# Kernel optimization log

Hardware: AMD Instinct MI355X
Metric: run time of the kernel (lower is better)

The kernel has to match this reference:

```python
import jax, jax.numpy as jnp
import numpy as np
import math

D = 1024      # hidden_size
H = 16        # num_heads
HD = D // H   # head_dim = 64
ROPE = 64     # rope_dim == head_dim (full-head rotation, empty pass-through)
E = 8         # num_experts
F = 2560
BASE = 10000.0
EPS = 1e-5
SPECIALS = jnp.arange(2, 8)  # special_tokens indices {2..7} used as global tokens


def _ln(x, w, b):
    m = x.mean(-1, keepdims=True)
    v = x.var(-1, keepdims=True)  # biased var, matches torch LayerNorm
    return (x - m) / jnp.sqrt(v + EPS) * w + b


def _rope(x, cos, sin):
    # x: [B,H,T,HD]; rotate first ROPE dims via half-split (NOT rotate-half interleave)
    x1, x2 = x[..., : ROPE // 2], x[..., ROPE // 2 : ROPE]
    rot = jnp.concatenate([x1 * cos - x2 * sin, x1 * sin + x2 * cos], axis=-1)
    return jnp.concatenate([rot, x[..., ROPE:]], axis=-1)


def setup_inputs() -> dict:
    key = jax.random.key(0)
    ks = jax.random.split(key, 8)
    B, T = 1, 1024
    g = lambda k, shape, s: (jax.random.normal(k, shape, jnp.float32) * s)
    return {
        "x": g(ks[0], (B, T, D), 1.0),
        "input_ids": jax.random.randint(ks[1], (B, T), 0, 32000),
        "ln1_w": jnp.ones((D,), jnp.float32), "ln1_b": jnp.zeros((D,), jnp.float32),
        "qkv_w": g(ks[2], (D, 3 * D), 0.02), "qkv_b": jnp.zeros((3 * D,), jnp.float32),
        "attn_out_w": g(ks[3], (D, D), 0.02), "attn_out_b": jnp.zeros((D,), jnp.float32),
        "ln2_w": jnp.ones((D,), jnp.float32), "ln2_b": jnp.zeros((D,), jnp.float32),
        "gate_w": g(ks[4], (D, E), 0.02), "gate_b": jnp.zeros((E,), jnp.float32),
        "fc_w": g(ks[5], (E, D, 2 * F), 0.02), "fc_b": jnp.zeros((E, 2 * F), jnp.float32),
        "eout_w": g(ks[6], (E, F, D), 0.02), "eout_b": jnp.zeros((E, D), jnp.float32),
    }


def _block(x, input_ids, ln1_w, ln1_b, qkv_w, qkv_b, attn_out_w, attn_out_b,
           ln2_w, ln2_b, gate_w, gate_b, fc_w, fc_b, eout_w, eout_b):
    B, T, _ = x.shape
    # --- self-attention (pre-norm) ---
    h = _ln(x, ln1_w, ln1_b)
    qkv = h @ qkv_w + qkv_b
    q, k, v = jnp.split(qkv, 3, axis=-1)
    resh = lambda t: t.reshape(B, T, H, HD).transpose(0, 2, 1, 3)  # [B,H,T,HD]
    q, k, v = resh(q), resh(k), resh(v)
    pos = jnp.arange(T, dtype=jnp.float32)
    inv = 1.0 / (BASE ** (jnp.arange(0, ROPE, 2, dtype=jnp.float32) / ROPE))
    fr = pos[:, None] * inv[None, :]            # [T, ROPE/2]
    cos, sin = jnp.cos(fr), jnp.sin(fr)
    q = _rope(q, cos, sin)
    k = _rope(k, cos, sin)
    causal = jnp.tril(jnp.ones((T, T), bool))
    glob = (input_ids[..., None] == SPECIALS).any(-1)            # [B,T]
    allowed = causal[None, None] | glob[:, None, :, None]        # [B,1,T,T]
    logits = jnp.einsum('bhqd,bhkd->bhqk', q, k) / math.sqrt(HD)
    neg = -jnp.finfo(logits.dtype).max
    logits = jnp.where(allowed, logits, neg)
    aw = jax.nn.softmax(logits, axis=-1)
    attn = jnp.einsum('bhqk,bhkd->bhqd', aw, v).transpose(0, 2, 1, 3).reshape(B, T, H * HD)
    x = x + (attn @ attn_out_w + attn_out_b)
    # --- MoE GEGLU FFN (hard top-1 routing) ---
    h2 = _ln(x, ln2_w, ln2_b)
    gp = jax.nn.softmax(h2 @ gate_w + gate_b, axis=-1)           # [B,T,E]
    gw = gp.max(-1)
    gi = gp.argmax(-1)
    xf = h2.reshape(-1, D)
    gif = gi.reshape(-1)
    gwf = gw.reshape(-1)
    N = xf.shape[0]
    outf = jnp.zeros((N, D), x.dtype)
    for e in range(E):  # fixed small expert loop; select by routing mask
        h12 = xf @ fc_w[e] + fc_b[e]
        x1, x2 = h12[:, :F], h12[:, F:]
        y = (x1 * jax.nn.gelu(x2, approximate=False)) @ eout_w[e] + eout_b[e]
        outf = outf + jnp.where((gif == e)[:, None], y, 0.0)
    outf = outf * gwf[:, None]
    sums = jax.ops.segment_sum(gwf, gif, num_segments=E)
    counts = jax.ops.segment_sum(jnp.ones_like(gwf), gif, num_segments=E)
    usage = sums / (counts + 1e-8)
    moe_loss = jnp.sum((usage - 1.0 / E) ** 2)
    return x + outf.reshape(B, T, D), moe_loss


def reference(x, input_ids, ln1_w, ln1_b, qkv_w, qkv_b, attn_out_w, attn_out_b,
              ln2_w, ln2_b, gate_w, gate_b, fc_w, fc_b, eout_w, eout_b):
    return _block(x, input_ids, ln1_w, ln1_b, qkv_w, qkv_b, attn_out_w, attn_out_b,
                  ln2_w, ln2_b, gate_w, gate_b, fc_w, fc_b, eout_w, eout_b)
```

## Files before the change

kernel.cpp:

```cpp
#include <hip/hip_runtime.h>
#include <float.h>
#include <math.h>
#include <stdint.h>

#define T_ 1024
#define D_ 1024
#define H_ 16
#define HD_ 64
#define E_ 8
#define F_ 2560
#define D3_ 3072
#define F2_ 5120

#define WS_H    0u
#define WS_QKV  1048576u
#define WS_ATTN 4194304u
#define WS_X2   5242880u
#define WS_H2   6291456u
#define WS_A    7340032u
#define WS_GW   9961472u
#define WS_GI   9962496u
#define WS_OFFS 9963520u
#define WS_PERM 9963536u

typedef short short8 __attribute__((ext_vector_type(8)));
typedef short short4v __attribute__((ext_vector_type(4)));
typedef __bf16 bf16x8 __attribute__((ext_vector_type(8)));
typedef float floatx4 __attribute__((ext_vector_type(4)));

union FragU { short8 s; bf16x8 b; };

__device__ __forceinline__ short f2bf(float f) {
    union { float f; uint32_t u; } a; a.f = f;
    uint32_t r = a.u + 0x7fffu + ((a.u >> 16) & 1u);
    return (short)(r >> 16);
}

__device__ __forceinline__ void cvt16(const float4& a0, const float4& a1,
                                      const float4& a2, const float4& a3,
                                      short8& c0, short8& c1) {
    c0[0]=f2bf(a0.x); c0[1]=f2bf(a0.y); c0[2]=f2bf(a0.z); c0[3]=f2bf(a0.w);
    c0[4]=f2bf(a1.x); c0[5]=f2bf(a1.y); c0[6]=f2bf(a1.z); c0[7]=f2bf(a1.w);
    c1[0]=f2bf(a2.x); c1[1]=f2bf(a2.y); c1[2]=f2bf(a2.z); c1[3]=f2bf(a2.w);
    c1[4]=f2bf(a3.x); c1[5]=f2bf(a3.y); c1[6]=f2bf(a3.z); c1[7]=f2bf(a3.w);
}

#define GEMM_IDS \
    const int tid  = threadIdx.x;                 \
    const int a_m  = tid >> 1;                    \
    const int a_kh = (tid & 1) * 16;              \
    const int lane = tid & 63, wave = tid >> 6;   \
    const int wm = wave & 1,  wn = wave >> 1;     \
    const int quad = lane >> 4, lm = lane & 15;

__global__ __launch_bounds__(256) void gemm_mfma_full(
    const float* __restrict__ A, int lda,
    const float* __restrict__ B, int ldb,
    const float* __restrict__ bias,
    float* __restrict__ C, int ldc, int K)
{
    __shared__ __align__(16) short As[4*128*8];
    __shared__ __align__(16) short Bs[64*40];
    const int row0 = blockIdx.y * 128, col0 = blockIdx.x * 64;
    GEMM_IDS
    const int b_n = tid >> 2, b_kc = tid & 3;
    floatx4 acc[4][2];
    #pragma unroll
    for (int i=0;i<4;i++)
        #pragma unroll
        for (int j=0;j<2;j++) acc[i][j] = (floatx4){0.f,0.f,0.f,0.f};

    const float* apx = A + (size_t)(row0 + a_m) * lda + a_kh;
    const float* bpx = B + (size_t)(b_kc*8) * ldb + col0 + b_n;
    const int kcA = (tid & 1) * 2;

    float4 a0, a1, a2, a3; float bvv[8];
    a0 = *(const float4*)(apx);     a1 = *(const float4*)(apx + 4);
    a2 = *(const float4*)(apx + 8); a3 = *(const float4*)(apx + 12);
    #pragma unroll
    for (int j=0;j<8;j++) bvv[j] = bpx[(size_t)j*ldb];

    for (int k0 = 0; k0 < K; k0 += 32) {
        __syncthreads();
        short8 c0, c1, cb;
        cvt16(a0,a1,a2,a3,c0,c1);
        #pragma unroll
        for (int j=0;j<8;j++) cb[j] = f2bf(bvv[j]);
        *(short8*)&As[((kcA  )*128 + a_m)*8] = c0;
        *(short8*)&As[((kcA+1)*128 + a_m)*8] = c1;
        *(short8*)&Bs[b_n*40 + b_kc*8] = cb;
        __syncthreads();
        if (k0 + 32 < K) {
            const float* ap2 = apx + k0 + 32;
            a0 = *(const float4*)(ap2);     a1 = *(const float4*)(ap2 + 4);
            a2 = *(const float4*)(ap2 + 8); a3 = *(const float4*)(ap2 + 12);
            const float* bp2 = bpx + (size_t)(k0+32) * ldb;
            #pragma unroll
            for (int j=0;j<8;j++) bvv[j] = bp2[(size_t)j*ldb];
        }
        FragU fa[4], fb[2];
        #pragma unroll
        for (int i=0;i<4;i++) fa[i].s = *(short8*)&As[(quad*128 + wm*64 + i*16 + lm)*8];
        #pragma unroll
        for (int j=0;j<2;j++) fb[j].s = *(short8*)&Bs[(wn*32 + j*16 + lm)*40 + quad*8];
        #pragma unroll
        for (int i=0;i<4;i++)
            #pragma unroll
            for (int j=0;j<2;j++)
                acc[i][j] = __builtin_amdgcn_mfma_f32_16x16x32_bf16(fa[i].b, fb[j].b, acc[i][j], 0,0,0);
    }
    #pragma unroll
    for (int i=0;i<4;i++)
        #pragma unroll
        for (int j=0;j<2;j++) {
            int col = col0 + wn*32 + j*16 + lm;
            float bb = bias ? bias[col] : 0.f;
            #pragma unroll
            for (int r=0;r<4;r++) {
                int row = row0 + wm*64 + i*16 + quad*4 + r;
                C[(size_t)row*ldc + col] = acc[i][j][r] + bb;
            }
        }
}

__global__ __launch_bounds__(256) void gemm_mfma_acc(
    const float* __restrict__ A, int lda,
    const float* __restrict__ B, int ldb, long sB,
    const int* __restrict__ offs, const int* __restrict__ perm,
    float* __restrict__ Cacc, int ldc, int K, int nsk)
{
    const int sk = blockIdx.z % nsk;
    const int e  = blockIdx.z / nsk;
    int off = 0, Ne = T_;
    if (offs) { off = offs[e]; Ne = offs[e+1] - off; }
    const int row0 = blockIdx.y * 128;
    if (row0 >= Ne) return;
    const int col0 = blockIdx.x * 64;
    B += (long)e * sB;

    __shared__ __align__(16) short As[4*128*8];
    __shared__ __align__(16) short Bs[64*40];
    __shared__ int toks[128];
    GEMM_IDS
    const int b_n = tid >> 2, b_kc = tid & 3;
    if (tid < 128) {
        int r = row0 + tid;
        toks[tid] = offs ? ((r < Ne) ? perm[off + r] : -1) : r;
    }
    __syncthreads();

    floatx4 acc[4][2];
    #pragma unroll
    for (int i=0;i<4;i++)
        #pragma unroll
        for (int j=0;j<2;j++) acc[i][j] = (floatx4){0.f,0.f,0.f,0.f};

    const int tokA = toks[a_m];
    const float* apx = (tokA >= 0) ? (A + (size_t)tokA * lda + a_kh) : nullptr;
    const float* bpx = B + (size_t)(b_kc*8) * ldb + col0 + b_n;
    const int kcA = (tid & 1) * 2;
    const int Kp = K / nsk;
    const int koff = sk * Kp, kend = koff + Kp;

    float4 a0, a1, a2, a3; float bvv[8];
    a0 = make_float4(0,0,0,0); a1 = a0; a2 = a0; a3 = a0;
    if (apx) {
        a0 = *(const float4*)(apx + koff);     a1 = *(const float4*)(apx + koff + 4);
        a2 = *(const float4*)(apx + koff + 8); a3 = *(const float4*)(apx + koff + 12);
    }
    {
        const float* bp2 = bpx + (size_t)koff * ldb;
        #pragma unroll
        for (int j=0;j<8;j++) bvv[j] = bp2[(size_t)j*ldb];
    }

    for (int k0 = koff; k0 < kend; k0 += 32) {
        __syncthreads();
        short8 c0, c1, cb;
        cvt16(a0,a1,a2,a3,c0,c1);
        #pragma unroll
        for (int j=0;j<8;j++) cb[j] = f2bf(bvv[j]);
        *(short8*)&As[((kcA  )*128 + a_m)*8] = c0;
        *(short8*)&As[((kcA+1)*128 + a_m)*8] = c1;
        *(short8*)&Bs[b_n*40 + b_kc*8] = cb;
        __syncthreads();
        if (k0 + 32 < kend) {
            if (apx) {
                const float* ap2 = apx + k0 + 32;
                a0 = *(const float4*)(ap2);     a1 = *(const float4*)(ap2 + 4);
                a2 = *(const float4*)(ap2 + 8); a3 = *(const float4*)(ap2 + 12);
            }
            const float* bp2 = bpx + (size_t)(k0+32) * ldb;
            #pragma unroll
            for (int j=0;j<8;j++) bvv[j] = bp2[(size_t)j*ldb];
        }
        FragU fa[4], fb[2];
        #pragma unroll
        for (int i=0;i<4;i++) fa[i].s = *(short8*)&As[(quad*128 + wm*64 + i*16 + lm)*8];
        #pragma unroll
        for (int j=0;j<2;j++) fb[j].s = *(short8*)&Bs[(wn*32 + j*16 + lm)*40 + quad*8];
        #pragma unroll
        for (int i=0;i<4;i++)
            #pragma unroll
            for (int j=0;j<2;j++)
                acc[i][j] = __builtin_amdgcn_mfma_f32_16x16x32_bf16(fa[i].b, fb[j].b, acc[i][j], 0,0,0);
    }
    #pragma unroll
    for (int i=0;i<4;i++)
        #pragma unroll
        for (int j=0;j<2;j++) {
            int col = col0 + wn*32 + j*16 + lm;
            #pragma unroll
            for (int r=0;r<4;r++) {
                int tk = toks[wm*64 + i*16 + quad*4 + r];
                if (tk >= 0) atomicAdd(&Cacc[(size_t)tk*ldc + col], acc[i][j][r]);
            }
        }
}

__global__ __launch_bounds__(256) void moe_fc_mfma(
    const float* __restrict__ h2, const float* __restrict__ fcw,
    const float* __restrict__ fcb, const int* __restrict__ offs,
    const int* __restrict__ perm, float* __restrict__ aout)
{
    const int e = blockIdx.z;
    const int off = offs[e];
    const int Ne = offs[e+1] - off;
    const int row0 = blockIdx.y * 128;
    if (row0 >= Ne) return;
    const int col0 = blockIdx.x * 32;

    __shared__ __align__(16) short As[4*128*8];
    __shared__ __align__(16) short B1s[32*40];
    __shared__ __align__(16) short B2s[32*40];
    __shared__ int toks[128];
    GEMM_IDS
    const int n_l = tid & 31, kg = tid >> 5;
    if (tid < 128) {
        int r = row0 + tid;
        toks[tid] = (r < Ne) ? perm[off + r] : -1;
    }
    __syncthreads();

    floatx4 acc1[4], acc2[4];
    #pragma unroll
    for (int i=0;i<4;i++) {
        acc1[i] = (floatx4){0.f,0.f,0.f,0.f};
        acc2[i] = (floatx4){0.f,0.f,0.f,0.f};
    }

    const float* W = fcw + (size_t)e * D_ * F2_;
    const int tokA = toks[a_m];
    const float* apx = (tokA >= 0) ? (h2 + (size_t)tokA * D_ + a_kh) : nullptr;
    const float* bpx = W + (size_t)(kg*4) * F2_ + col0 + n_l;
    const int kcA = (tid & 1) * 2;

    float4 a0, a1, a2, a3; float b1v[4], b2v[4];
    a0 = make_float4(0,0,0,0); a1 = a0; a2 = a0; a3 = a0;
    if (apx) {
        a0 = *(const float4*)(apx);     a1 = *(const float4*)(apx + 4);
        a2 = *(const float4*)(apx + 8); a3 = *(const float4*)(apx + 12);
    }
    #pragma unroll
    for (int j=0;j<4;j++) { b1v[j] = bpx[(size_t)j*F2_]; b2v[j] = bpx[(size_t)j*F2_ + F_]; }

    for (int k0 = 0; k0 < D_; k0 += 32) {
        __syncthreads();
        short8 c0, c1;
        short4v cb1, cb2;
        cvt16(a0,a1,a2,a3,c0,c1);
        #pragma unroll
        for (int j=0;j<4;j++) { cb1[j] = f2bf(b1v[j]); cb2[j] = f2bf(b2v[j]); }
        *(short8*)&As[((kcA  )*128 + a_m)*8] = c0;
        *(short8*)&As[((kcA+1)*128 + a_m)*8] = c1;
        *(short4v*)&B1s[n_l*40 + kg*4] = cb1;
        *(short4v*)&B2s[n_l*40 + kg*4] = cb2;
        __syncthreads();
        if (k0 + 32 < D_) {
            if (apx) {
                const float* ap2 = apx + k0 + 32;
                a0 = *(const float4*)(ap2);     a1 = *(const float4*)(ap2 + 4);
                a2 = *(const float4*)(ap2 + 8); a3 = *(const float4*)(ap2 + 12);
            }
            const float* bp2 = bpx + (size_t)(k0+32) * F2_;
            #pragma unroll
            for (int j=0;j<4;j++) { b1v[j] = bp2[(size_t)j*F2_]; b2v[j] = bp2[(size_t)j*F2_ + F_]; }
        }
        FragU fa[4], fb1, fb2;
        #pragma unroll
        for (int i=0;i<4;i++) fa[i].s = *(short8*)&As[(quad*128 + wm*64 + i*16 + lm)*8];
        fb1.s = *(short8*)&B1s[(wn*16 + lm)*40 + quad*8];
        fb2.s = *(short8*)&B2s[(wn*16 + lm)*40 + quad*8];
        #pragma unroll
        for (int i=0;i<4;i++) {
            acc1[i] = __builtin_amdgcn_mfma_f32_16x16x32_bf16(fa[i].b, fb1.b, acc1[i], 0,0,0);
            acc2[i] = __builtin_amdgcn_mfma_f32_16x16x32_bf16(fa[i].b, fb2.b, acc2[i], 0,0,0);
        }
    }
    {
        int col = col0 + wn*16 + lm;
        float b1 = fcb[(size_t)e*F2_ + col];
        float b2 = fcb[(size_t)e*F2_ + F_ + col];
        #pragma unroll
        for (int i=0;i<4;i++)
            #pragma unroll
            for (int r=0;r<4;r++) {
                int tk = toks[wm*64 + i*16 + quad*4 + r];
                if (tk < 0) continue;
                float v1 = acc1[i][r] + b1;
                float v2 = acc2[i][r] + b2;
                float g = v2 * 0.5f * (1.0f + erff(v2 * 0.70710678118654752f));
                aout[(size_t)tk*F_ + col] = v1 * g;
            }
    }
}

__global__ __launch_bounds__(128) void flash_attn(
    const float* __restrict__ qkv, const int* __restrict__ ids,
    float* __restrict__ attnout)
{
    const int h  = blockIdx.y;
    const int q0 = blockIdx.x * 32;
    const int tid = threadIdx.x;
    const int lane = tid & 63, w = tid >> 6;
    const int quad = lane >> 4, lm = lane & 15;

    __shared__ __align__(16) short Qs[32*72];
    __shared__ __align__(16) short Ks[64*72];
    __shared__ __align__(16) short Vt[64*72];
    __shared__ __align__(16) short Ps[2][16*72];
    __shared__ int globf[32];

    {
        int row = tid >> 2, c = (tid & 3) * 16;
        const float* qp = qkv + (size_t)(q0 + row) * D3_ + h * HD_ + c;
        float4 f0 = *(const float4*)(qp);
        float4 f1 = *(const float4*)(qp + 4);
        float4 f2 = *(const float4*)(qp + 8);
        float4 f3 = *(const float4*)(qp + 12);
        short8 s0, s1;
        cvt16(f0, f1, f2, f3, s0, s1);
        *(short8*)&Qs[row*72 + c]     = s0;
        *(short8*)&Qs[row*72 + c + 8] = s1;
    }
    if (tid < 32) {
        int id = ids[q0 + tid];
        globf[tid] = (id >= 2 && id <= 7) ? 1 : 0;
    }
    __syncthreads();

    FragU QA[2];
    #pragma unroll
    for (int s = 0; s < 2; s++)
        QA[s].s = *(short8*)&Qs[(w*16 + lm)*72 + s*32 + quad*8];

    int any = 0;
    #pragma unroll
    for (int i = 0; i < 32; i++) any |= globf[i];
    const int nt = any ? (T_/64) : ((q0 + 31) >> 6) + 1;

    int gq[4]; int qidx[4];
    #pragma unroll
    for (int r = 0; r < 4; r++) {
        int ql = w*16 + quad*4 + r;
        qidx[r] = q0 + ql;
        gq[r] = globf[ql];
    }

    float mrow[4] = {-1e30f, -1e30f, -1e30f, -1e30f};
    float lrow[4] = {0.f, 0.f, 0.f, 0.f};
    floatx4 Oacc[4];
    #pragma unroll
    for (int n = 0; n < 4; n++) Oacc[n] = (floatx4){0.f, 0.f, 0.f, 0.f};

    for (int kt = 0; kt < nt; kt++) {
        __syncthreads();
        #pragma unroll
        for (int rep = 0; rep < 2; rep++) {
            int key = (tid >> 2) + rep*32;
            int c = (tid & 3) * 16;
            const float* kp = qkv + (size_t)(kt*64 + key) * D3_ + D_ + h*HD_ + c;
            float4 f0 = *(const float4*)(kp);
            float4 f1 = *(const float4*)(kp + 4);
            float4 f2 = *(const float4*)(kp + 8);
            float4 f3 = *(const float4*)(kp + 12);
            short8 s0, s1;
            cvt16(f0, f1, f2, f3, s0, s1);
            *(short8*)&Ks[key*72 + c]     = s0;
            *(short8*)&Ks[key*72 + c + 8] = s1;
        }
        #pragma unroll
        for (int rep = 0; rep < 8; rep++) {
            int lin = tid + rep*128;
            int key = lin >> 4;
            int c = (lin & 15) * 4;
            const float* vp = qkv + (size_t)(kt*64 + key) * D3_ + 2*D_ + h*HD_ + c;
            float4 f = *(const float4*)vp;
            Vt[(c+0)*72 + key] = f2bf(f.x);
            Vt[(c+1)*72 + key] = f2bf(f.y);
            Vt[(c+2)*72 + key] = f2bf(f.z);
            Vt[(c+3)*72 + key] = f2bf(f.w);
        }
        __syncthreads();

        floatx4 Sv[4];
        #pragma unroll
        for (int n = 0; n < 4; n++) {
            Sv[n] = (floatx4){0.f, 0.f, 0.f, 0.f};
            #pragma unroll
            for (int s = 0; s < 2; s++) {
                FragU KB;
                KB.s = *(short8*)&Ks[(n*16 + lm)*72 + s*32 + quad*8];
                Sv[n] = __builtin_amdgcn_mfma_f32_16x16x32_bf16(QA[s].b, KB.b, Sv[n], 0, 0, 0);
            }
        }
        #pragma unroll
        for (int n = 0; n < 4; n++) {
            int key = kt*64 + n*16 + lm;
            #pragma unroll
            for (int r = 0; r < 4; r++) {
                float v = Sv[n][r] * 0.125f;
                if (!gq[r] && key > qidx[r]) v = -1e30f;
                Sv[n][r] = v;
            }
        }
        float mnew[4], alpha[4], tsum[4];
        #pragma unroll
        for (int r = 0; r < 4; r++) {
            float tm = fmaxf(fmaxf(Sv[0][r], Sv[1][r]), fmaxf(Sv[2][r], Sv[3][r]));
            #pragma unroll
            for (int x = 1; x < 16; x <<= 1) tm = fmaxf(tm, __shfl_xor(tm, x));
            mnew[r] = fmaxf(mrow[r], tm);
            alpha[r] = __expf(mrow[r] - mnew[r]);
            mrow[r] = mnew[r];
            tsum[r] = 0.f;
        }
        #pragma unroll
        for (int n = 0; n < 4; n++) {
            #pragma unroll
            for (int r = 0; r < 4; r++) {
                float p = __expf(Sv[n][r] - mnew[r]);
                tsum[r] += p;
                Ps[w][(quad*4 + r)*72 + n*16 + lm] = f2bf(p);
            }
        }
        #pragma unroll
        for (int r = 0; r < 4; r++) {
            #pragma unroll
            for (int x = 1; x < 16; x <<= 1) tsum[r] += __shfl_xor(tsum[r], x);
            lrow[r] = lrow[r] * alpha[r] + tsum[r];
        }
        #pragma unroll
        for (int n = 0; n < 4; n++)
            #pragma unroll
            for (int r = 0; r < 4; r++) Oacc[n][r] *= alpha[r];

        #pragma unroll
        for (int s = 0; s < 2; s++) {
            FragU PA;
            PA.s = *(short8*)&Ps[w][lm*72 + s*32 + quad*8];
            #pragma unroll
            for (int n = 0; n < 4; n++) {
                FragU VB;
                VB.s = *(short8*)&Vt[(n*16 + lm)*72 + s*32 + quad*8];
                Oacc[n] = __builtin_amdgcn_mfma_f32_16x16x32_bf16(PA.b, VB.b, Oacc[n], 0, 0, 0);
            }
        }
    }

    #pragma unroll
    for (int n = 0; n < 4; n++)
        #pragma unroll
        for (int r = 0; r < 4; r++) {
            float o = Oacc[n][r] / lrow[r];
            attnout[(size_t)qidx[r]*D_ + h*HD_ + n*16 + lm] = o;
        }
}

__global__ __launch_bounds__(256) void ep_attn(
    const float* __restrict__ x, const float* __restrict__ sacc,
    const float* __restrict__ aob, float* __restrict__ x2)
{
    int row = blockIdx.x, tid = threadIdx.x;
    float4 xv = ((const float4*)(x + (size_t)row*D_))[tid];
    float4 sv = ((const float4*)(sacc + (size_t)row*D_))[tid];
    float4 bv = ((const float4*)aob)[tid];
    float4 o;
    o.x = xv.x + sv.x + bv.x; o.y = xv.y + sv.y + bv.y;
    o.z = xv.z + sv.z + bv.z; o.w = xv.w + sv.w + bv.w;
    ((float4*)(x2 + (size_t)row*D_))[tid] = o;
}

__global__ __launch_bounds__(256) void ep_moe(
    const float* __restrict__ x2, const float* __restrict__ sacc,
    const float* __restrict__ eob, const float* __restrict__ gw,
    const int* __restrict__ gi, float* __restrict__ out)
{
    int row = blockIdx.x, tid = threadIdx.x;
    float g = gw[row];
    int e = gi[row];
    float4 xv = ((const float4*)(x2 + (size_t)row*D_))[tid];
    float4 sv = ((const float4*)(sacc + (size_t)row*D_))[tid];
    float4 bv = ((const float4*)(eob + (size_t)e*D_))[tid];
    float4 o;
    o.x = xv.x + g*(sv.x + bv.x); o.y = xv.y + g*(sv.y + bv.y);
    o.z = xv.z + g*(sv.z + bv.z); o.w = xv.w + g*(sv.w + bv.w);
    ((float4*)(out + (size_t)row*D_))[tid] = o;
}

__global__ __launch_bounds__(256) void ln_kernel(
    const float* __restrict__ x, const float* __restrict__ w,
    const float* __restrict__ b, float* __restrict__ out)
{
    const int row = blockIdx.x, tid = threadIdx.x;
    const int lane = tid & 63, wave = tid >> 6;
    float4 v = ((const float4*)(x + (size_t)row * D_))[tid];
    float s  = v.x + v.y + v.z + v.w;
    float sq = v.x*v.x + v.y*v.y + v.z*v.z + v.w*v.w;
    #pragma unroll
    for (int off = 32; off; off >>= 1) {
        s  += __shfl_down(s, off);
        sq += __shfl_down(sq, off);
    }
    __shared__ float rs[4], rq[4], mv[2];
    if (lane == 0) { rs[wave] = s; rq[wave] = sq; }
    __syncthreads();
    if (tid == 0) {
        float ts = rs[0]+rs[1]+rs[2]+rs[3];
        float tq = rq[0]+rq[1]+rq[2]+rq[3];
        float mean = ts * (1.0f / D_);
        float var  = tq * (1.0f / D_) - mean*mean;
        mv[0] = mean; mv[1] = rsqrtf(var + 1e-5f);
    }
    __syncthreads();
    float mean = mv[0], rstd = mv[1];
    float4 wv = ((const float4*)w)[tid];
    float4 bv = ((const float4*)b)[tid];
    float4 o;
    o.x = (v.x-mean)*rstd*wv.x + bv.x;
    o.y = (v.y-mean)*rstd*wv.y + bv.y;
    o.z = (v.z-mean)*rstd*wv.z + bv.z;
    o.w = (v.w-mean)*rstd*wv.w + bv.w;
    ((float4*)(out + (size_t)row * D_))[tid] = o;
}

__global__ __launch_bounds__(256) void rope_kernel(float* __restrict__ qkv)
{
    int gid = blockIdx.x * 256 + threadIdx.x;
    int t = gid >> 9;
    int r = gid & 511;
    int h = r >> 5;
    int d = r & 31;
    float inv = powf(10000.0f, -(float)d * (1.0f/32.0f));
    float fr = (float)t * inv;
    float s, c;
    sincosf(fr, &s, &c);
    float* base = qkv + (size_t)t*D3_ + h*HD_ + d;
    float q1 = base[0], q2 = base[32];
    base[0]  = q1*c - q2*s;
    base[32] = q1*s + q2*c;
    float* kb = base + D_;
    float k1 = kb[0], k2 = kb[32];
    kb[0]  = k1*c - k2*s;
    kb[32] = k1*s + k2*c;
}

__global__ __launch_bounds__(256) void ln2_gate_kernel(
    const float* __restrict__ x2, const float* __restrict__ w,
    const float* __restrict__ b, const float* __restrict__ gwm,
    const float* __restrict__ gbv, float* __restrict__ h2,
    int* __restrict__ gi, float* __restrict__ gw)
{
    const int row = blockIdx.x, tid = threadIdx.x;
    const int lane = tid & 63, wave = tid >> 6;
    float4 v = ((const float4*)(x2 + (size_t)row * D_))[tid];
    float s  = v.x + v.y + v.z + v.w;
    float sq = v.x*v.x + v.y*v.y + v.z*v.z + v.w*v.w;
    #pragma unroll
    for (int off = 32; off; off >>= 1) {
        s  += __shfl_down(s, off);
        sq += __shfl_down(sq, off);
    }
    __shared__ float rs[4], rq[4], mv[2];
    if (lane == 0) { rs[wave] = s; rq[wave] = sq; }
    __syncthreads();
    if (tid == 0) {
        float ts = rs[0]+rs[1]+rs[2]+rs[3];
        float tq = rq[0]+rq[1]+rq[2]+rq[3];
        float mean = ts * (1.0f / D_);
        float var  = tq * (1.0f / D_) - mean*mean;
        mv[0] = mean; mv[1] = rsqrtf(var + 1e-5f);
    }
    __syncthreads();
    float mean = mv[0], rstd = mv[1];
    float4 wv = ((const float4*)w)[tid];
    float4 bv = ((const float4*)b)[tid];
    float hv[4];
    hv[0] = (v.x-mean)*rstd*wv.x + bv.x;
    hv[1] = (v.y-mean)*rstd*wv.y + bv.y;
    hv[2] = (v.z-mean)*rstd*wv.z + bv.z;
    hv[3] = (v.w-mean)*rstd*wv.w + bv.w;
    float4 o; o.x=hv[0]; o.y=hv[1]; o.z=hv[2]; o.w=hv[3];
    ((float4*)(h2 + (size_t)row * D_))[tid] = o;

    float acc[E_] = {};
    int c = tid * 4;
    #pragma unroll
    for (int j = 0; j < 4; j++) {
        const float* gr = gwm + (size_t)(c+j) * E_;
        #pragma unroll
        for (int e = 0; e < E_; e++) acc[e] += hv[j] * gr[e];
    }
    #pragma unroll
    for (int off = 32; off; off >>= 1)
        #pragma unroll
        for (int e = 0; e < E_; e++) acc[e] += __shfl_down(acc[e], off);
    __shared__ float gred[4][E_];
    if (lane == 0)
        for (int e = 0; e < E_; e++) gred[wave][e] = acc[e];
    __syncthreads();
    if (tid == 0) {
        float lg[E_];
        float mxl = -FLT_MAX; int mi = 0;
        for (int e = 0; e < E_; e++)
            lg[e] = gred[0][e]+gred[1][e]+gred[2][e]+gred[3][e] + gbv[e];
        for (int e = 0; e < E_; e++)
            if (lg[e] > mxl) { mxl = lg[e]; mi = e; }
        float ssum = 0.f;
        for (int e = 0; e < E_; e++) ssum += expf(lg[e] - mxl);
        gi[row] = mi;
        gw[row] = 1.0f / ssum;
    }
}

__global__ void route_kernel(const int* __restrict__ gi,
                             int* __restrict__ offs, int* __restrict__ perm)
{
    __shared__ int cnt[E_], c2[E_], off[E_+1];
    const int tid = threadIdx.x;
    if (tid < E_) { cnt[tid] = 0; c2[tid] = 0; }
    __syncthreads();
    int e = gi[tid];
    atomicAdd(&cnt[e], 1);
    __syncthreads();
    if (tid == 0) {
        off[0] = 0;
        for (int i = 0; i < E_; i++) off[i+1] = off[i] + cnt[i];
        for (int i = 0; i <= E_; i++) offs[i] = off[i];
    }
    __syncthreads();
    int r = atomicAdd(&c2[e], 1);
    perm[off[e] + r] = tid;
}

__global__ void loss_kernel(const int* __restrict__ gi,
                            const float* __restrict__ gw, float* __restrict__ out)
{
    __shared__ float ss[E_], sc[E_];
    const int tid = threadIdx.x;
    if (tid < E_) { ss[tid] = 0.f; sc[tid] = 0.f; }
    __syncthreads();
    for (int t = tid; t < T_; t += 256) {
        int e = gi[t];
        atomicAdd(&ss[e], gw[t]);
        atomicAdd(&sc[e], 1.0f);
    }
    __syncthreads();
    if (tid == 0) {
        float loss = 0.f;
        for (int e = 0; e < E_; e++) {
            float u = ss[e] / (sc[e] + 1e-8f);
            float d = u - 0.125f;
            loss += d * d;
        }
        out[(size_t)T_ * D_] = loss;
    }
}

extern "C" void kernel_launch(void* const* d_in, const int* in_sizes, int n_in,
                              void* d_out, int out_size, void* d_ws, size_t ws_size,
                              hipStream_t stream)
{
    const float* x     = (const float*)d_in[0];
    const int*   ids   = (const int*)d_in[1];
    const float* ln1w  = (const float*)d_in[2];
    const float* ln1b  = (const float*)d_in[3];
    const float* qkvw  = (const float*)d_in[4];
    const float* qkvb  = (const float*)d_in[5];
    const float* aow   = (const float*)d_in[6];
    const float* aob   = (const float*)d_in[7];
    const float* ln2w  = (const float*)d_in[8];
    const float* ln2b  = (const float*)d_in[9];
    const float* gatew = (const float*)d_in[10];
    const float* gateb = (const float*)d_in[11];
    const float* fcw   = (const float*)d_in[12];
    const float* fcb   = (const float*)d_in[13];
    const float* eoutw = (const float*)d_in[14];
    const float* eoutb = (const float*)d_in[15];
    float* out = (float*)d_out;
    float* ws  = (float*)d_ws;

    float* h    = ws + WS_H;
    float* sacc = ws + WS_H;
    float* qkv  = ws + WS_QKV;
    float* attn = ws + WS_ATTN;
    float* x2   = ws + WS_X2;
    float* h2   = ws + WS_H2;
    float* abuf = ws + WS_A;
    float* gw   = ws + WS_GW;
    int*   gi   = (int*)(ws + WS_GI);
    int*   offs = (int*)(ws + WS_OFFS);
    int*   perm = (int*)(ws + WS_PERM);

    ln_kernel<<<T_, 256, 0, stream>>>(x, ln1w, ln1b, h);
    gemm_mfma_full<<<dim3(D3_/64, T_/128), 256, 0, stream>>>(
        h, D_, qkvw, D3_, qkvb, qkv, D3_, D_);
    rope_kernel<<<(T_*H_*32)/256, 256, 0, stream>>>(qkv);
    flash_attn<<<dim3(T_/32, H_), 128, 0, stream>>>(qkv, ids, attn);
    hipMemsetAsync(sacc, 0, (size_t)T_*D_*sizeof(float), stream);
    gemm_mfma_acc<<<dim3(D_/64, T_/128, 4), 256, 0, stream>>>(
        attn, D_, aow, D_, 0, nullptr, nullptr, sacc, D_, D_, 4);
    ep_attn<<<T_, 256, 0, stream>>>(x, sacc, aob, x2);
    ln2_gate_kernel<<<T_, 256, 0, stream>>>(x2, ln2w, ln2b, gatew, gateb, h2, gi, gw);
    route_kernel<<<1, T_, 0, stream>>>(gi, offs, perm);
    moe_fc_mfma<<<dim3(F_/32, T_/128, E_), 256, 0, stream>>>(h2, fcw, fcb, offs, perm, abuf);
    hipMemsetAsync(sacc, 0, (size_t)T_*D_*sizeof(float), stream);
    gemm_mfma_acc<<<dim3(D_/64, T_/128, 4*E_), 256, 0, stream>>>(
        abuf, F_, eoutw, D_, (long)F_*D_, offs, perm, sacc, D_, F_, 4);
    ep_moe<<<T_, 256, 0, stream>>>(x2, sacc, eoutb, gw, gi, out);
    loss_kernel<<<1, 256, 0, stream>>>(gi, gw, out);
}
```

Baseline: 592.6 us.

## Swap GEMM operand roles so weights are staged in LDS and tokens read directly

Adds 'swapped' GEMM kernels for the QKV projection and both MoE expert GEMMs. Each block stages a 64-column weight tile as bf16 in shared memory and reads 128 token rows straight from global memory into MFMA fragments. Outputs go through an LDS transpose so global stores are coalesced. The MoE output GEMM now writes four split-K partial buffers that the epilogue sums, replacing the memset plus atomicAdd scheme. The cost is that activation fragments are reloaded from global or L2 with no LDS reuse, and the partial buffers add extra memory traffic.

```diff
diff --git a/kernel.cpp b/kernel.cpp
--- a/kernel.cpp
+++ b/kernel.cpp
@@ -22,9 +22,9 @@
 #define WS_GI   9962496u
 #define WS_OFFS 9963520u
 #define WS_PERM 9963536u
+#define WS_PART 0u
 
 typedef short short8 __attribute__((ext_vector_type(8)));
-typedef short short4v __attribute__((ext_vector_type(4)));
 typedef __bf16 bf16x8 __attribute__((ext_vector_type(8)));
 typedef float floatx4 __attribute__((ext_vector_type(4)));
 
@@ -45,6 +45,299 @@
     c1[4]=f2bf(a3.x); c1[5]=f2bf(a3.y); c1[6]=f2bf(a3.z); c1[7]=f2bf(a3.w);
 }
 
+__device__ __forceinline__ void bfrag(const float* p, FragU& f) {
+    float4 f0 = *(const float4*)p;
+    float4 f1 = *(const float4*)(p + 4);
+    f.s[0]=f2bf(f0.x); f.s[1]=f2bf(f0.y); f.s[2]=f2bf(f0.z); f.s[3]=f2bf(f0.w);
+    f.s[4]=f2bf(f1.x); f.s[5]=f2bf(f1.y); f.s[6]=f2bf(f1.z); f.s[7]=f2bf(f1.w);
+}
+
+
+#define SW_IDS \
+    const int tid = threadIdx.x;                   \
+    const int lane = tid & 63, wave = tid >> 6;    \
+    const int wm = wave & 1, wn = wave >> 1;       \
+    const int quad = lane >> 4, lm = lane & 15;    \
+    const int krp = tid >> 4, mseg = tid & 15;     \
+    const int kc_w = krp >> 2, jd = krp & 3;
+
+#define SW_PACK(P0, P1, AU) {                                              \
+    _Pragma("unroll")                                                      \
+    for (int c = 0; c < 4; c++) {                                          \
+        uint32_t v = (uint32_t)(unsigned short)f2bf(((const float*)&P0)[c])\
+              | ((uint32_t)(unsigned short)f2bf(((const float*)&P1)[c]) << 16); \
+        AU[(kc_w*64 + mseg*4 + c)*4 + jd] = v;                             \
+    } }
+
+__global__ __launch_bounds__(256) void qkv_sw(
+    const float* __restrict__ h, const float* __restrict__ qkvw,
+    const float* __restrict__ qkvb, float* __restrict__ qkv)
+{
+    const int n0 = blockIdx.x * 128;
+    const int m0 = blockIdx.y * 64;
+
+    __shared__ __align__(16) short As[4*64*8];
+    __shared__ __align__(16) float Ct[128*68];
+    SW_IDS
+
+    int btok[4];
+    #pragma unroll
+    for (int j = 0; j < 4; j++) btok[j] = n0 + wn*64 + j*16 + lm;
+
+    floatx4 acc[2][4];
+    #pragma unroll
+    for (int i=0;i<2;i++)
+        #pragma unroll
+        for (int j=0;j<4;j++) acc[i][j] = (floatx4){0.f,0.f,0.f,0.f};
+
+    const float* Wb = qkvw + (size_t)(2*krp)*D3_ + m0 + mseg*4;
+    float4 p0 = *(const float4*)(Wb);
+    float4 p1 = *(const float4*)(Wb + D3_);
+
+    for (int k0 = 0; k0 < D_; k0 += 32) {
+        __syncthreads();
+        uint32_t* Au = (uint32_t*)As;
+        SW_PACK(p0, p1, Au)
+        __syncthreads();
+        if (k0 + 32 < D_) {
+            const float* Wn = Wb + (size_t)(k0+32)*D3_;
+            p0 = *(const float4*)(Wn);
+            p1 = *(const float4*)(Wn + D3_);
+        }
+        FragU fb[4];
+        #pragma unroll
+        for (int j = 0; j < 4; j++)
+            bfrag(h + (size_t)btok[j]*D_ + k0 + quad*8, fb[j]);
+        FragU fa[2];
+        #pragma unroll
+        for (int i = 0; i < 2; i++)
+            fa[i].s = *(short8*)&As[(quad*64 + wm*32 + i*16 + lm)*8];
+        #pragma unroll
+        for (int i = 0; i < 2; i++)
+            #pragma unroll
+            for (int j = 0; j < 4; j++)
+                acc[i][j] = __builtin_amdgcn_mfma_f32_16x16x32_bf16(fa[i].b, fb[j].b, acc[i][j], 0,0,0);
+    }
+    #pragma unroll
+    for (int i = 0; i < 2; i++)
+        #pragma unroll
+        for (int r = 0; r < 4; r++) {
+            int colL = wm*32 + i*16 + quad*4 + r;
+            float bb = qkvb[m0 + colL];
+            #pragma unroll
+            for (int j = 0; j < 4; j++)
+                Ct[(wn*64 + j*16 + lm)*68 + colL] = acc[i][j][r] + bb;
+        }
+    __syncthreads();
+    {
+        int row = tid >> 1, half = tid & 1;
+        float* op = qkv + (size_t)(n0 + row)*D3_ + m0 + half*32;
+        const float* cp = &Ct[row*68 + half*32];
+        #pragma unroll
+        for (int i = 0; i < 8; i++)
+            *(float4*)(op + i*4) = *(const float4*)(cp + i*4);
+    }
+}
+
+__global__ __launch_bounds__(256) void moe_fc_sw(
+    const float* __restrict__ h2, const float* __restrict__ fcw,
+    const float* __restrict__ fcb, const int* __restrict__ offs,
+    const int* __restrict__ perm, float* __restrict__ aout)
+{
+    const int e = blockIdx.z;
+    const int off = offs[e], Ne = offs[e+1] - off;
+    const int n0 = blockIdx.x * 128;
+    if (n0 >= Ne) return;
+    const int m0 = blockIdx.y * 64;
+
+    __shared__ __align__(16) short As1[4*64*8];
+    __shared__ __align__(16) short As2[4*64*8];
+    __shared__ __align__(16) float Ct[128*68];
+    __shared__ int toks[128];
+    SW_IDS
+
+    if (tid < 128) {
+        int r = n0 + tid;
+        toks[tid] = (r < Ne) ? perm[off + r] : -1;
+    }
+    __syncthreads();
+
+    int btok[4];
+    #pragma unroll
+    for (int j = 0; j < 4; j++) btok[j] = toks[wn*64 + j*16 + lm];
+
+    floatx4 acc1[2][4], acc2[2][4];
+    #pragma unroll
+    for (int i=0;i<2;i++)
+        #pragma unroll
+        for (int j=0;j<4;j++) {
+            acc1[i][j] = (floatx4){0.f,0.f,0.f,0.f};
+            acc2[i][j] = (floatx4){0.f,0.f,0.f,0.f};
+        }
+
+    const float* W1 = fcw + (size_t)e*D_*F2_ + (size_t)(2*krp)*F2_ + m0 + mseg*4;
+    const float* W2 = W1 + F_;
+    float4 p10 = *(const float4*)(W1);
+    float4 p11 = *(const float4*)(W1 + F2_);
+    float4 p20 = *(const float4*)(W2);
+    float4 p21 = *(const float4*)(W2 + F2_);
+
+    for (int k0 = 0; k0 < D_; k0 += 32) {
+        __syncthreads();
+        uint32_t* A1u = (uint32_t*)As1;
+        uint32_t* A2u = (uint32_t*)As2;
+        SW_PACK(p10, p11, A1u)
+        SW_PACK(p20, p21, A2u)
+        __syncthreads();
+        if (k0 + 32 < D_) {
+            const float* W1n = W1 + (size_t)(k0+32)*F2_;
+            p10 = *(const float4*)(W1n);
+            p11 = *(const float4*)(W1n + F2_);
+            const float* W2n = W2 + (size_t)(k0+32)*F2_;
+            p20 = *(const float4*)(W2n);
+            p21 = *(const float4*)(W2n + F2_);
+        }
+        FragU fb[4];
+        #pragma unroll
+        for (int j = 0; j < 4; j++) {
+            if (btok[j] >= 0)
+                bfrag(h2 + (size_t)btok[j]*D_ + k0 + quad*8, fb[j]);
+            else
+                fb[j].s = (short8){0,0,0,0,0,0,0,0};
+        }
+        FragU fa1[2], fa2[2];
+        #pragma unroll
+        for (int i = 0; i < 2; i++) {
+            fa1[i].s = *(short8*)&As1[(quad*64 + wm*32 + i*16 + lm)*8];
+            fa2[i].s = *(short8*)&As2[(quad*64 + wm*32 + i*16 + lm)*8];
+        }
+        #pragma unroll
+        for (int i = 0; i < 2; i++)
+            #pragma unroll
+            for (int j = 0; j < 4; j++) {
+                acc1[i][j] = __builtin_amdgcn_mfma_f32_16x16x32_bf16(fa1[i].b, fb[j].b, acc1[i][j], 0,0,0);
+                acc2[i][j] = __builtin_amdgcn_mfma_f32_16x16x32_bf16(fa2[i].b, fb[j].b, acc2[i][j], 0,0,0);
+            }
+    }
+    #pragma unroll
+    for (int i = 0; i < 2; i++)
+        #pragma unroll
+        for (int r = 0; r < 4; r++) {
+            int colL = wm*32 + i*16 + quad*4 + r;
+            float b1 = fcb[(size_t)e*F2_ + m0 + colL];
+            float b2 = fcb[(size_t)e*F2_ + F_ + m0 + colL];
+            #pragma unroll
+            for (int j = 0; j < 4; j++) {
+                float v1 = acc1[i][j][r] + b1;
+                float v2 = acc2[i][j][r] + b2;
+                float g = v2 * 0.5f * (1.0f + erff(v2 * 0.70710678118654752f));
+                Ct[(wn*64 + j*16 + lm)*68 + colL] = v1 * g;
+            }
+        }
+    __syncthreads();
+    {
+        int row = tid >> 1, half = tid & 1;
+        int tk = toks[row];
+        if (tk >= 0) {
+            float* op = aout + (size_t)tk*F_ + m0 + half*32;
+            const float* cp = &Ct[row*68 + half*32];
+            #pragma unroll
+            for (int i = 0; i < 8; i++)
+                *(float4*)(op + i*4) = *(const float4*)(cp + i*4);
+        }
+    }
+}
+
+__global__ __launch_bounds__(256) void moe_out_sw(
+    const float* __restrict__ abuf, const float* __restrict__ ew,
+    const int* __restrict__ offs, const int* __restrict__ perm,
+    float* __restrict__ part)
+{
+    const int e = blockIdx.z >> 2;
+    const int sk = blockIdx.z & 3;
+    const int off = offs[e], Ne = offs[e+1] - off;
+    const int n0 = blockIdx.x * 128;
+    if (n0 >= Ne) return;
+    const int m0 = blockIdx.y * 64;
+
+    __shared__ __align__(16) short As[4*64*8];
+    __shared__ __align__(16) float Ct[128*68];
+    __shared__ int toks[128];
+    SW_IDS
+
+    if (tid < 128) {
+        int r = n0 + tid;
+        toks[tid] = (r < Ne) ? perm[off + r] : -1;
+    }
+    __syncthreads();
+
+    int btok[4];
+    #pragma unroll
+    for (int j = 0; j < 4; j++) btok[j] = toks[wn*64 + j*16 + lm];
+
+    floatx4 acc[2][4];
+    #pragma unroll
+    for (int i=0;i<2;i++)
+        #pragma unroll
+        for (int j=0;j<4;j++) acc[i][j] = (floatx4){0.f,0.f,0.f,0.f};
+
+    const int koff = sk * (F_ / 4);
+    const int kend = koff + (F_ / 4);
+    const float* Wb = ew + (size_t)e*F_*D_ + (size_t)(koff + 2*krp)*D_ + m0 + mseg*4;
+    float4 p0 = *(const float4*)(Wb);
+    float4 p1 = *(const float4*)(Wb + D_);
+
+    for (int k0 = koff; k0 < kend; k0 += 32) {
+        __syncthreads();
+        uint32_t* Au = (uint32_t*)As;
+        SW_PACK(p0, p1, Au)
+        __syncthreads();
+        if (k0 + 32 < kend) {
+            const float* Wn = Wb + (size_t)(k0 + 32 - koff)*D_;
+            p0 = *(const float4*)(Wn);
+            p1 = *(const float4*)(Wn + D_);
+        }
+        FragU fb[4];
+        #pragma unroll
+        for (int j = 0; j < 4; j++) {
+            if (btok[j] >= 0)
+                bfrag(abuf + (size_t)btok[j]*F_ + k0 + quad*8, fb[j]);
+            else
+                fb[j].s = (short8){0,0,0,0,0,0,0,0};
+        }
+        FragU fa[2];
+        #pragma unroll
+        for (int i = 0; i < 2; i++)
+            fa[i].s = *(short8*)&As[(quad*64 + wm*32 + i*16 + lm)*8];
+        #pragma unroll
+        for (int i = 0; i < 2; i++)
+            #pragma unroll
+            for (int j = 0; j < 4; j++)
+                acc[i][j] = __builtin_amdgcn_mfma_f32_16x16x32_bf16(fa[i].b, fb[j].b, acc[i][j], 0,0,0);
+    }
+    #pragma unroll
+    for (int i = 0; i < 2; i++)
+        #pragma unroll
+        for (int r = 0; r < 4; r++) {
+            int colL = wm*32 + i*16 + quad*4 + r;
+            #pragma unroll
+            for (int j = 0; j < 4; j++)
+                Ct[(wn*64 + j*16 + lm)*68 + colL] = acc[i][j][r];
+        }
+    __syncthreads();
+    {
+        int row = tid >> 1, half = tid & 1;
+        int tk = toks[row];
+        if (tk >= 0) {
+            float* op = part + (size_t)sk*T_*D_ + (size_t)tk*D_ + m0 + half*32;
+            const float* cp = &Ct[row*68 + half*32];
+            #pragma unroll
+            for (int i = 0; i < 8; i++)
+                *(float4*)(op + i*4) = *(const float4*)(cp + i*4);
+        }
+    }
+}
+
 #define GEMM_IDS \
     const int tid  = threadIdx.x;                 \
     const int a_m  = tid >> 1;                    \
@@ -53,17 +346,20 @@
     const int wm = wave & 1,  wn = wave >> 1;     \
     const int quad = lane >> 4, lm = lane & 15;
 
-__global__ __launch_bounds__(256) void gemm_mfma_full(
+__global__ __launch_bounds__(256) void gemm_mfma_acc(
     const float* __restrict__ A, int lda,
     const float* __restrict__ B, int ldb,
-    const float* __restrict__ bias,
-    float* __restrict__ C, int ldc, int K)
-{
+    float* __restrict__ Cacc, int ldc, int K, int nsk)
+{
+    const int sk = blockIdx.z;
+    const int row0 = blockIdx.y * 128;
+    const int col0 = blockIdx.x * 64;
+
     __shared__ __align__(16) short As[4*128*8];
     __shared__ __align__(16) short Bs[64*40];
-    const int row0 = blockIdx.y * 128, col0 = blockIdx.x * 64;
     GEMM_IDS
     const int b_n = tid >> 2, b_kc = tid & 3;
+
     floatx4 acc[4][2];
     #pragma unroll
     for (int i=0;i<4;i++)
@@ -73,14 +369,19 @@
     const float* apx = A + (size_t)(row0 + a_m) * lda + a_kh;
     const float* bpx = B + (size_t)(b_kc*8) * ldb + col0 + b_n;
     const int kcA = (tid & 1) * 2;
+    const int Kp = K / nsk;
+    const int koff = sk * Kp, kend = koff + Kp;
 
     float4 a0, a1, a2, a3; float bvv[8];
-    a0 = *(const float4*)(apx);     a1 = *(const float4*)(apx + 4);
-    a2 = *(const float4*)(apx + 8); a3 = *(const float4*)(apx + 12);
-    #pragma unroll
-    for (int j=0;j<8;j++) bvv[j] = bpx[(size_t)j*ldb];
-
-    for (int k0 = 0; k0 < K; k0 += 32) {
+    a0 = *(const float4*)(apx + koff);     a1 = *(const float4*)(apx + koff + 4);
+    a2 = *(const float4*)(apx + koff + 8); a3 = *(const float4*)(apx + koff + 12);
+    {
+        const float* bp2 = bpx + (size_t)koff * ldb;
+        #pragma unroll
+        for (int j=0;j<8;j++) bvv[j] = bp2[(size_t)j*ldb];
+    }
+
+    for (int k0 = koff; k0 < kend; k0 += 32) {
         __syncthreads();
         short8 c0, c1, cb;
         cvt16(a0,a1,a2,a3,c0,c1);
@@ -90,7 +391,7 @@
         *(short8*)&As[((kcA+1)*128 + a_m)*8] = c1;
         *(short8*)&Bs[b_n*40 + b_kc*8] = cb;
         __syncthreads();
-        if (k0 + 32 < K) {
+        if (k0 + 32 < kend) {
             const float* ap2 = apx + k0 + 32;
             a0 = *(const float4*)(ap2);     a1 = *(const float4*)(ap2 + 4);
             a2 = *(const float4*)(ap2 + 8); a3 = *(const float4*)(ap2 + 12);
@@ -114,205 +415,12 @@
         #pragma unroll
         for (int j=0;j<2;j++) {
             int col = col0 + wn*32 + j*16 + lm;
-            float bb = bias ? bias[col] : 0.f;
             #pragma unroll
             for (int r=0;r<4;r++) {
                 int row = row0 + wm*64 + i*16 + quad*4 + r;
-                C[(size_t)row*ldc + col] = acc[i][j][r] + bb;
+                atomicAdd(&Cacc[(size_t)row*ldc + col], acc[i][j][r]);
             }
         }
-}
-
-__global__ __launch_bounds__(256) void gemm_mfma_acc(
-    const float* __restrict__ A, int lda,
-    const float* __restrict__ B, int ldb, long sB,
-    const int* __restrict__ offs, const int* __restrict__ perm,
-    float* __restrict__ Cacc, int ldc, int K, int nsk)
-{
-    const int sk = blockIdx.z % nsk;
-    const int e  = blockIdx.z / nsk;
-    int off = 0, Ne = T_;
-    if (offs) { off = offs[e]; Ne = offs[e+1] - off; }
-    const int row0 = blockIdx.y * 128;
-    if (row0 >= Ne) return;
-    const int col0 = blockIdx.x * 64;
-    B += (long)e * sB;
-
-    __shared__ __align__(16) short As[4*128*8];
-    __shared__ __align__(16) short Bs[64*40];
-    __shared__ int toks[128];
-    GEMM_IDS
-    const int b_n = tid >> 2, b_kc = tid & 3;
-    if (tid < 128) {
-        int r = row0 + tid;
-        toks[tid] = offs ? ((r < Ne) ? perm[off + r] : -1) : r;
-    }
-    __syncthreads();
-
-    floatx4 acc[4][2];
-    #pragma unroll
-    for (int i=0;i<4;i++)
-        #pragma unroll
-        for (int j=0;j<2;j++) acc[i][j] = (floatx4){0.f,0.f,0.f,0.f};
-
-    const int tokA = toks[a_m];
-    const float* apx = (tokA >= 0) ? (A + (size_t)tokA * lda + a_kh) : nullptr;
-    const float* bpx = B + (size_t)(b_kc*8) * ldb + col0 + b_n;
-    const int kcA = (tid & 1) * 2;
-    const int Kp = K / nsk;
-    const int koff = sk * Kp, kend = koff + Kp;
-
-    float4 a0, a1, a2, a3; float bvv[8];
-    a0 = make_float4(0,0,0,0); a1 = a0; a2 = a0; a3 = a0;
-    if (apx) {
-        a0 = *(const float4*)(apx + koff);     a1 = *(const float4*)(apx + koff + 4);
-        a2 = *(const float4*)(apx + koff + 8); a3 = *(const float4*)(apx + koff + 12);
-    }
-    {
-        const float* bp2 = bpx + (size_t)koff * ldb;
-        #pragma unroll
-        for (int j=0;j<8;j++) bvv[j] = bp2[(size_t)j*ldb];
-    }
-
-    for (int k0 = koff; k0 < kend; k0 += 32) {
-        __syncthreads();
-        short8 c0, c1, cb;
-        cvt16(a0,a1,a2,a3,c0,c1);
-        #pragma unroll
-        for (int j=0;j<8;j++) cb[j] = f2bf(bvv[j]);
-        *(short8*)&As[((kcA  )*128 + a_m)*8] = c0;
-        *(short8*)&As[((kcA+1)*128 + a_m)*8] = c1;
-        *(short8*)&Bs[b_n*40 + b_kc*8] = cb;
-        __syncthreads();
-        if (k0 + 32 < kend) {
-            if (apx) {
-                const float* ap2 = apx + k0 + 32;
-                a0 = *(const float4*)(ap2);     a1 = *(const float4*)(ap2 + 4);
-                a2 = *(const float4*)(ap2 + 8); a3 = *(const float4*)(ap2 + 12);
-            }
-            const float* bp2 = bpx + (size_t)(k0+32) * ldb;
-            #pragma unroll
-            for (int j=0;j<8;j++) bvv[j] = bp2[(size_t)j*ldb];
-        }
-        FragU fa[4], fb[2];
-        #pragma unroll
-        for (int i=0;i<4;i++) fa[i].s = *(short8*)&As[(quad*128 + wm*64 + i*16 + lm)*8];
-        #pragma unroll
-        for (int j=0;j<2;j++) fb[j].s = *(short8*)&Bs[(wn*32 + j*16 + lm)*40 + quad*8];
-        #pragma unroll
-        for (int i=0;i<4;i++)
-            #pragma unroll
-            for (int j=0;j<2;j++)
-                acc[i][j] = __builtin_amdgcn_mfma_f32_16x16x32_bf16(fa[i].b, fb[j].b, acc[i][j], 0,0,0);
-    }
-    #pragma unroll
-    for (int i=0;i<4;i++)
-        #pragma unroll
-        for (int j=0;j<2;j++) {
-            int col = col0 + wn*32 + j*16 + lm;
-            #pragma unroll
-            for (int r=0;r<4;r++) {
-                int tk = toks[wm*64 + i*16 + quad*4 + r];
-                if (tk >= 0) atomicAdd(&Cacc[(size_t)tk*ldc + col], acc[i][j][r]);
-            }
-        }
-}
-
-__global__ __launch_bounds__(256) void moe_fc_mfma(
-    const float* __restrict__ h2, const float* __restrict__ fcw,
-    const float* __restrict__ fcb, const int* __restrict__ offs,
-    const int* __restrict__ perm, float* __restrict__ aout)
-{
-    const int e = blockIdx.z;
-    const int off = offs[e];
-    const int Ne = offs[e+1] - off;
-    const int row0 = blockIdx.y * 128;
-    if (row0 >= Ne) return;
-    const int col0 = blockIdx.x * 32;
-
-    __shared__ __align__(16) short As[4*128*8];
-    __shared__ __align__(16) short B1s[32*40];
-    __shared__ __align__(16) short B2s[32*40];
-    __shared__ int toks[128];
-    GEMM_IDS
-    const int n_l = tid & 31, kg = tid >> 5;
-    if (tid < 128) {
-        int r = row0 + tid;
-        toks[tid] = (r < Ne) ? perm[off + r] : -1;
-    }
-    __syncthreads();
-
-    floatx4 acc1[4], acc2[4];
-    #pragma unroll
-    for (int i=0;i<4;i++) {
-        acc1[i] = (floatx4){0.f,0.f,0.f,0.f};
-        acc2[i] = (floatx4){0.f,0.f,0.f,0.f};
-    }
-
-    const float* W = fcw + (size_t)e * D_ * F2_;
-    const int tokA = toks[a_m];
-    const float* apx = (tokA >= 0) ? (h2 + (size_t)tokA * D_ + a_kh) : nullptr;
-    const float* bpx = W + (size_t)(kg*4) * F2_ + col0 + n_l;
-    const int kcA = (tid & 1) * 2;
-
-    float4 a0, a1, a2, a3; float b1v[4], b2v[4];
-    a0 = make_float4(0,0,0,0); a1 = a0; a2 = a0; a3 = a0;
-    if (apx) {
-        a0 = *(const float4*)(apx);     a1 = *(const float4*)(apx + 4);
-        a2 = *(const float4*)(apx + 8); a3 = *(const float4*)(apx + 12);
-    }
-    #pragma unroll
-    for (int j=0;j<4;j++) { b1v[j] = bpx[(size_t)j*F2_]; b2v[j] = bpx[(size_t)j*F2_ + F_]; }
-
-    for (int k0 = 0; k0 < D_; k0 += 32) {
-        __syncthreads();
-        short8 c0, c1;
-        short4v cb1, cb2;
-        cvt16(a0,a1,a2,a3,c0,c1);
-        #pragma unroll
-        for (int j=0;j<4;j++) { cb1[j] = f2bf(b1v[j]); cb2[j] = f2bf(b2v[j]); }
-        *(short8*)&As[((kcA  )*128 + a_m)*8] = c0;
-        *(short8*)&As[((kcA+1)*128 + a_m)*8] = c1;
-        *(short4v*)&B1s[n_l*40 + kg*4] = cb1;
-        *(short4v*)&B2s[n_l*40 + kg*4] = cb2;
-        __syncthreads();
-        if (k0 + 32 < D_) {
-            if (apx) {
-                const float* ap2 = apx + k0 + 32;
-                a0 = *(const float4*)(ap2);     a1 = *(const float4*)(ap2 + 4);
-                a2 = *(const float4*)(ap2 + 8); a3 = *(const float4*)(ap2 + 12);
-            }
-            const float* bp2 = bpx + (size_t)(k0+32) * F2_;
-            #pragma unroll
-            for (int j=0;j<4;j++) { b1v[j] = bp2[(size_t)j*F2_]; b2v[j] = bp2[(size_t)j*F2_ + F_]; }
-        }
-        FragU fa[4], fb1, fb2;
-        #pragma unroll
-        for (int i=0;i<4;i++) fa[i].s = *(short8*)&As[(quad*128 + wm*64 + i*16 + lm)*8];
-        fb1.s = *(short8*)&B1s[(wn*16 + lm)*40 + quad*8];
-        fb2.s = *(short8*)&B2s[(wn*16 + lm)*40 + quad*8];
-        #pragma unroll
-        for (int i=0;i<4;i++) {
-            acc1[i] = __builtin_amdgcn_mfma_f32_16x16x32_bf16(fa[i].b, fb1.b, acc1[i], 0,0,0);
-            acc2[i] = __builtin_amdgcn_mfma_f32_16x16x32_bf16(fa[i].b, fb2.b, acc2[i], 0,0,0);
-        }
-    }
-    {
-        int col = col0 + wn*16 + lm;
-        float b1 = fcb[(size_t)e*F2_ + col];
-        float b2 = fcb[(size_t)e*F2_ + F_ + col];
-        #pragma unroll
-        for (int i=0;i<4;i++)
-            #pragma unroll
-            for (int r=0;r<4;r++) {
-                int tk = toks[wm*64 + i*16 + quad*4 + r];
-                if (tk < 0) continue;
-                float v1 = acc1[i][r] + b1;
-                float v2 = acc2[i][r] + b2;
-                float g = v2 * 0.5f * (1.0f + erff(v2 * 0.70710678118654752f));
-                aout[(size_t)tk*F_ + col] = v1 * g;
-            }
-    }
 }
 
 __global__ __launch_bounds__(128) void flash_attn(
@@ -491,8 +599,8 @@
     ((float4*)(x2 + (size_t)row*D_))[tid] = o;
 }
 
-__global__ __launch_bounds__(256) void ep_moe(
-    const float* __restrict__ x2, const float* __restrict__ sacc,
+__global__ __launch_bounds__(256) void ep_moe2(
+    const float* __restrict__ x2, const float* __restrict__ part,
     const float* __restrict__ eob, const float* __restrict__ gw,
     const int* __restrict__ gi, float* __restrict__ out)
 {
@@ -500,11 +608,16 @@
     float g = gw[row];
     int e = gi[row];
     float4 xv = ((const float4*)(x2 + (size_t)row*D_))[tid];
-    float4 sv = ((const float4*)(sacc + (size_t)row*D_))[tid];
+    float4 s0 = ((const float4*)(part + 0ul*T_*D_ + (size_t)row*D_))[tid];
+    float4 s1 = ((const float4*)(part + 1ul*T_*D_ + (size_t)row*D_))[tid];
+    float4 s2 = ((const float4*)(part + 2ul*T_*D_ + (size_t)row*D_))[tid];
+    float4 s3 = ((const float4*)(part + 3ul*T_*D_ + (size_t)row*D_))[tid];
     float4 bv = ((const float4*)(eob + (size_t)e*D_))[tid];
     float4 o;
-    o.x = xv.x + g*(sv.x + bv.x); o.y = xv.y + g*(sv.y + bv.y);
-    o.z = xv.z + g*(sv.z + bv.z); o.w = xv.w + g*(sv.w + bv.w);
+    o.x = xv.x + g*(s0.x+s1.x+s2.x+s3.x + bv.x);
+    o.y = xv.y + g*(s0.y+s1.y+s2.y+s3.y + bv.y);
+    o.z = xv.z + g*(s0.z+s1.z+s2.z+s3.z + bv.z);
+    o.w = xv.w + g*(s0.w+s1.w+s2.w+s3.w + bv.w);
     ((float4*)(out + (size_t)row*D_))[tid] = o;
 }
 
@@ -702,6 +815,7 @@
 
     float* h    = ws + WS_H;
     float* sacc = ws + WS_H;
+    float* part = ws + WS_PART;
     float* qkv  = ws + WS_QKV;
     float* attn = ws + WS_ATTN;
     float* x2   = ws + WS_X2;
@@ -713,20 +827,17 @@
     int*   perm = (int*)(ws + WS_PERM);
 
     ln_kernel<<<T_, 256, 0, stream>>>(x, ln1w, ln1b, h);
-    gemm_mfma_full<<<dim3(D3_/64, T_/128), 256, 0, stream>>>(
-        h, D_, qkvw, D3_, qkvb, qkv, D3_, D_);
+    qkv_sw<<<dim3(8, 48), 256, 0, stream>>>(h, qkvw, qkvb, qkv);
     rope_kernel<<<(T_*H_*32)/256, 256, 0, stream>>>(qkv);
     flash_attn<<<dim3(T_/32, H_), 128, 0, stream>>>(qkv, ids, attn);
     hipMemsetAsync(sacc, 0, (size_t)T_*D_*sizeof(float), stream);
     gemm_mfma_acc<<<dim3(D_/64, T_/128, 4), 256, 0, stream>>>(
-        attn, D_, aow, D_, 0, nullptr, nullptr, sacc, D_, D_, 4);
+        attn, D_, aow, D_, sacc, D_, D_, 4);
     ep_attn<<<T_, 256, 0, stream>>>(x, sacc, aob, x2);
     ln2_gate_kernel<<<T_, 256, 0, stream>>>(x2, ln2w, ln2b, gatew, gateb, h2, gi, gw);
     route_kernel<<<1, T_, 0, stream>>>(gi, offs, perm);
-    moe_fc_mfma<<<dim3(F_/32, T_/128, E_), 256, 0, stream>>>(h2, fcw, fcb, offs, perm, abuf);
-    hipMemsetAsync(sacc, 0, (size_t)T_*D_*sizeof(float), stream);
-    gemm_mfma_acc<<<dim3(D_/64, T_/128, 4*E_), 256, 0, stream>>>(
-        abuf, F_, eoutw, D_, (long)F_*D_, offs, perm, sacc, D_, F_, 4);
-    ep_moe<<<T_, 256, 0, stream>>>(x2, sacc, eoutb, gw, gi, out);
+    moe_fc_sw<<<dim3(8, F_/64, E_), 256, 0, stream>>>(h2, fcw, fcb, offs, perm, abuf);
+    moe_out_sw<<<dim3(8, D_/64, 4*E_), 256, 0, stream>>>(abuf, eoutw, offs, perm, part);
+    ep_moe2<<<T_, 256, 0, stream>>>(x2, part, eoutb, gw, gi, out);
     loss_kernel<<<1, 256, 0, stream>>>(gi, gw, out);
 }
```

New measurement: 1.310 ms. 2.21x slower.
